# Performance work log

Hardware: AMD Instinct MI355X
Metric: run time of the kernel (lower is better)

Reference implementation:

```python
import jax, jax.numpy as jnp
import numpy as np

LAMBDA = 1.0

def _patches3x3(x):
    # x: [B, C, H, W] -> [B, C, 3, 3, H, W] of 3x3 zero-padded neighborhoods
    B, C, H, W = x.shape
    xp = jnp.pad(x, ((0, 0), (0, 0), (1, 1), (1, 1)))
    rows = []
    for i in range(3):
        cols = [xp[:, :, i:i + H, j:j + W] for j in range(3)]
        rows.append(jnp.stack(cols, axis=2))  # [B, C, 3, H, W]
    return jnp.stack(rows, axis=2)  # [B, C, 3, 3, H, W]


def setup_inputs() -> dict:
    key = jax.random.key(0)
    kU, kV, kW = jax.random.split(key, 3)
    B, Cin, Cout, H, W = 8, 16, 16, 224, 224
    U = jax.random.normal(kU, (B, Cin, H, W), dtype=jnp.float32)
    V = jax.random.normal(kV, (B, Cin, H, W), dtype=jnp.float32)
    # nn.init.uniform_(weight, -0.1, 0.1)
    weight = jax.random.uniform(kW, (Cout, Cin, 3, 3), dtype=jnp.float32,
                                minval=-0.1, maxval=0.1)
    return {"U": U, "V": V, "weight": weight}


def reference(U, V, weight):
    # u1_u2 / v1_v2: 3x3 neighborhood minus center pixel, per input channel
    u_diff = _patches3x3(U) - U[:, :, None, None, :, :]  # [B,C,3,3,H,W]
    v_diff = _patches3x3(V) - V[:, :, None, None, :, :]
    inv_l2 = 1.0 / (LAMBDA * LAMBDA)
    # S = 1 / sqrt(1 + |v1-v2|^2 / lambda^2)
    S = jax.lax.rsqrt(1.0 + v_diff * v_diff * inv_l2)
    # out[b,o,h,w] = sum_{c,ki,kj} weight[o,c,ki,kj] * S * u_diff
    out = jnp.einsum('ocij,bcijhw->bohw', weight, S * u_diff)
    return out
```

## Files before the change

kernel.cpp:

```cpp
#include <hip/hip_runtime.h>


constexpr int Bn = 8, Ci = 16, Co = 16, H = 224, W = 224;
constexpr int HW = H * W;
constexpr int TW = 32, TH = 8;

template <bool EDGE>
__device__ __forceinline__ void load_nbhd(const float* __restrict__ p,
                                          int h, int w, float out9[9]) {
#pragma unroll
  for (int dh = 0; dh < 3; ++dh) {
#pragma unroll
    for (int dw = 0; dw < 3; ++dw) {
      const int k = dh * 3 + dw;
      if (!EDGE) {
        out9[k] = p[(dh - 1) * W + (dw - 1)];
      } else {
        const int hh = h + dh - 1, ww = w + dw - 1;
        const bool ok = ((unsigned)hh < (unsigned)H) & ((unsigned)ww < (unsigned)W);
        const int off = ok ? ((dh - 1) * W + (dw - 1)) : 0;
        const float val = p[off];
        out9[k] = ok ? val : 0.0f;
      }
    }
  }
}

template <bool EDGE>
__device__ __forceinline__ void compute_pixel(
    const float* __restrict__ U, const float* __restrict__ V,
    float* __restrict__ Out, int b, int h, int w,
    const float (*__restrict__ wt)[9][Co]) {
  float acc[Co];
#pragma unroll
  for (int o = 0; o < Co; ++o) acc[o] = 0.0f;

  const size_t pix = (size_t)h * W + w;
  const float* up0 = U + (size_t)b * Ci * HW + pix;
  const float* vp0 = V + (size_t)b * Ci * HW + pix;

  for (int c = 0; c < Ci; ++c) {
    const float* up = up0 + c * HW;
    const float* vp = vp0 + c * HW;
    float u[9], v[9];
    load_nbhd<EDGE>(up, h, w, u);
    load_nbhd<EDGE>(vp, h, w, v);
    const float uc = u[4], vc = v[4];

    float t[9];
#pragma unroll
    for (int k = 0; k < 9; ++k) {
      if (k == 4) continue;
      const float vd = v[k] - vc;
      const float s = rsqrtf(fmaf(vd, vd, 1.0f));
      t[k] = s * (u[k] - uc);
    }

#pragma unroll
    for (int k = 0; k < 9; ++k) {
      if (k == 4) continue;
      const float tk = t[k];
#pragma unroll
      for (int o = 0; o < Co; o += 4) {
        const float4 wv = *reinterpret_cast<const float4*>(&wt[c][k][o]);
        acc[o + 0] = fmaf(wv.x, tk, acc[o + 0]);
        acc[o + 1] = fmaf(wv.y, tk, acc[o + 1]);
        acc[o + 2] = fmaf(wv.z, tk, acc[o + 2]);
        acc[o + 3] = fmaf(wv.w, tk, acc[o + 3]);
      }
    }
  }

  float* op = Out + (size_t)b * Co * HW + pix;
#pragma unroll
  for (int o = 0; o < Co; ++o) op[(size_t)o * HW] = acc[o];
}

__global__ __launch_bounds__(256)
void sdconv_kernel(const float* __restrict__ U, const float* __restrict__ V,
                   const float* __restrict__ Wg, float* __restrict__ Out) {
  __shared__ float wt[Ci][9][Co];
  for (int i = threadIdx.x; i < Co * Ci * 9; i += 256) {
    const int k = i % 9;
    const int c = (i / 9) % Ci;
    const int o = i / (9 * Ci);
    wt[c][k][o] = Wg[i];
  }
  __syncthreads();

  const int tw = threadIdx.x & (TW - 1);
  const int th = threadIdx.x / TW;
  const int w = blockIdx.x * TW + tw;
  const int h = blockIdx.y * TH + th;
  const int b = blockIdx.z;

  const bool edge = (blockIdx.x == 0) | (blockIdx.x == gridDim.x - 1) |
                    (blockIdx.y == 0) | (blockIdx.y == gridDim.y - 1);
  if (edge)
    compute_pixel<true>(U, V, Out, b, h, w, wt);
  else
    compute_pixel<false>(U, V, Out, b, h, w, wt);
}

extern "C" void kernel_launch(void* const* d_in, const int* in_sizes, int n_in,
                              void* d_out, int out_size, void* d_ws, size_t ws_size,
                              hipStream_t stream) {
  const float* U  = (const float*)d_in[0];
  const float* V  = (const float*)d_in[1];
  const float* Wg = (const float*)d_in[2];
  float* Out = (float*)d_out;

  dim3 grid(W / TW, H / TH, Bn);
  dim3 block(TW * TH);
  sdconv_kernel<<<grid, block, 0, stream>>>(U, V, Wg, Out);
}
```

Before: 134.5 us.

## Compute channel-tap contraction with fp16 MFMA and sliding-row neighborhood reuse

Replaces the per-pixel scalar FMA loop over 16 output channels with a 16x16x32 fp16 MFMA per row of pixels. The 8 non-center taps times 4 channels per lane group form the K dimension. Each wave computes 16 pixels by 4 rows, sliding a 3-row window so vertical neighbor loads are reused across rows. Weights are loaded straight from global memory into fp16 B fragments, with no shared-memory staging. This trades fp32 accuracy for fp16 operands and gives a smaller block and tile.

```diff
diff --git a/kernel.cpp b/kernel.cpp
--- a/kernel.cpp
+++ b/kernel.cpp
@@ -3,103 +3,118 @@
 
 constexpr int Bn = 8, Ci = 16, Co = 16, H = 224, W = 224;
 constexpr int HW = H * W;
-constexpr int TW = 32, TH = 8;
+
+typedef _Float16 f16x8 __attribute__((ext_vector_type(8)));
+typedef float    f32x4 __attribute__((ext_vector_type(4)));
 
 template <bool EDGE>
-__device__ __forceinline__ void load_nbhd(const float* __restrict__ p,
-                                          int h, int w, float out9[9]) {
-#pragma unroll
-  for (int dh = 0; dh < 3; ++dh) {
-#pragma unroll
-    for (int dw = 0; dw < 3; ++dw) {
-      const int k = dh * 3 + dw;
-      if (!EDGE) {
-        out9[k] = p[(dh - 1) * W + (dw - 1)];
-      } else {
-        const int hh = h + dh - 1, ww = w + dw - 1;
-        const bool ok = ((unsigned)hh < (unsigned)H) & ((unsigned)ww < (unsigned)W);
-        const int off = ok ? ((dh - 1) * W + (dw - 1)) : 0;
-        const float val = p[off];
-        out9[k] = ok ? val : 0.0f;
-      }
+__device__ __forceinline__ void load_row(const float* __restrict__ plane,
+                                         int h, int w, float r[3]) {
+  if (!EDGE) {
+    const float* q = plane + h * W + w;
+    r[0] = q[-1]; r[1] = q[0]; r[2] = q[1];
+  } else {
+    if ((unsigned)h < (unsigned)H) {
+      const float* q = plane + h * W + w;
+      r[0] = (w >= 1)     ? q[-1] : 0.0f;
+      r[1] = q[0];
+      r[2] = (w + 1 < W) ? q[1] : 0.0f;
+    } else {
+      r[0] = 0.0f; r[1] = 0.0f; r[2] = 0.0f;
     }
   }
 }
 
 template <bool EDGE>
-__device__ __forceinline__ void compute_pixel(
+__device__ __forceinline__ void sdconv_wave(
     const float* __restrict__ U, const float* __restrict__ V,
-    float* __restrict__ Out, int b, int h, int w,
-    const float (*__restrict__ wt)[9][Co]) {
-  float acc[Co];
+    const float* __restrict__ Wg, float* __restrict__ Out,
+    int b, int h0, int w0, int lane) {
+  const int px = lane & 15;
+  const int cg = lane >> 4;
+
+  const int w = w0 + px;
+
+  f16x8 bfrag[4];
 #pragma unroll
-  for (int o = 0; o < Co; ++o) acc[o] = 0.0f;
+  for (int kc = 0; kc < 4; ++kc) {
+    const int c = 4 * kc + cg;
+    const float* wp = Wg + (px * Ci + c) * 9;
+#pragma unroll
+    for (int j = 0; j < 8; ++j) {
+      const int tap = (j < 4) ? j : j + 1;
+      bfrag[kc][j] = (_Float16)wp[tap];
+    }
+  }
 
-  const size_t pix = (size_t)h * W + w;
-  const float* up0 = U + (size_t)b * Ci * HW + pix;
-  const float* vp0 = V + (size_t)b * Ci * HW + pix;
-
-  for (int c = 0; c < Ci; ++c) {
-    const float* up = up0 + c * HW;
-    const float* vp = vp0 + c * HW;
-    float u[9], v[9];
-    load_nbhd<EDGE>(up, h, w, u);
-    load_nbhd<EDGE>(vp, h, w, v);
-    const float uc = u[4], vc = v[4];
-
-    float t[9];
+  f32x4 d[4];
 #pragma unroll
-    for (int k = 0; k < 9; ++k) {
-      if (k == 4) continue;
-      const float vd = v[k] - vc;
-      const float s = rsqrtf(fmaf(vd, vd, 1.0f));
-      t[k] = s * (u[k] - uc);
-    }
+  for (int r = 0; r < 4; ++r) { d[r][0] = 0.f; d[r][1] = 0.f; d[r][2] = 0.f; d[r][3] = 0.f; }
 
 #pragma unroll
-    for (int k = 0; k < 9; ++k) {
-      if (k == 4) continue;
-      const float tk = t[k];
+  for (int kc = 0; kc < 4; ++kc) {
+    const int c = 4 * kc + cg;
+    const float* up = U + ((size_t)(b * Ci + c)) * HW;
+    const float* vp = V + ((size_t)(b * Ci + c)) * HW;
+
+    float u[3][3], v[3][3];
+    load_row<EDGE>(up, h0 - 1, w, u[0]);
+    load_row<EDGE>(vp, h0 - 1, w, v[0]);
+    load_row<EDGE>(up, h0,     w, u[1]);
+    load_row<EDGE>(vp, h0,     w, v[1]);
+
 #pragma unroll
-      for (int o = 0; o < Co; o += 4) {
-        const float4 wv = *reinterpret_cast<const float4*>(&wt[c][k][o]);
-        acc[o + 0] = fmaf(wv.x, tk, acc[o + 0]);
-        acc[o + 1] = fmaf(wv.y, tk, acc[o + 1]);
-        acc[o + 2] = fmaf(wv.z, tk, acc[o + 2]);
-        acc[o + 3] = fmaf(wv.w, tk, acc[o + 3]);
+    for (int r = 0; r < 4; ++r) {
+      load_row<EDGE>(up, h0 + r + 1, w, u[2]);
+      load_row<EDGE>(vp, h0 + r + 1, w, v[2]);
+
+      const float uc = u[1][1], vc = v[1][1];
+      f16x8 a;
+      int j = 0;
+#pragma unroll
+      for (int dh = 0; dh < 3; ++dh) {
+#pragma unroll
+        for (int dw = 0; dw < 3; ++dw) {
+          if (dh == 1 && dw == 1) continue;
+          const float vd = v[dh][dw] - vc;
+          const float s  = rsqrtf(fmaf(vd, vd, 1.0f));
+          a[j++] = (_Float16)(s * (u[dh][dw] - uc));
+        }
+      }
+      d[r] = __builtin_amdgcn_mfma_f32_16x16x32_f16(a, bfrag[kc], d[r], 0, 0, 0);
+
+#pragma unroll
+      for (int i = 0; i < 3; ++i) {
+        u[0][i] = u[1][i]; u[1][i] = u[2][i];
+        v[0][i] = v[1][i]; v[1][i] = v[2][i];
       }
     }
   }
 
-  float* op = Out + (size_t)b * Co * HW + pix;
+  const int wst = w0 + 4 * cg;
+  const int o   = px;
 #pragma unroll
-  for (int o = 0; o < Co; ++o) op[(size_t)o * HW] = acc[o];
+  for (int r = 0; r < 4; ++r) {
+    float* op = Out + (((size_t)b * Co + o) * H + (h0 + r)) * W + wst;
+    *reinterpret_cast<f32x4*>(op) = d[r];
+  }
 }
 
-__global__ __launch_bounds__(256)
-void sdconv_kernel(const float* __restrict__ U, const float* __restrict__ V,
-                   const float* __restrict__ Wg, float* __restrict__ Out) {
-  __shared__ float wt[Ci][9][Co];
-  for (int i = threadIdx.x; i < Co * Ci * 9; i += 256) {
-    const int k = i % 9;
-    const int c = (i / 9) % Ci;
-    const int o = i / (9 * Ci);
-    wt[c][k][o] = Wg[i];
-  }
-  __syncthreads();
-
-  const int tw = threadIdx.x & (TW - 1);
-  const int th = threadIdx.x / TW;
-  const int w = blockIdx.x * TW + tw;
-  const int h = blockIdx.y * TH + th;
-  const int b = blockIdx.z;
+__global__ __launch_bounds__(128)
+void sdconv_mfma(const float* __restrict__ U, const float* __restrict__ V,
+                 const float* __restrict__ Wg, float* __restrict__ Out) {
+  const int lane = threadIdx.x & 63;
+  const int wv   = threadIdx.x >> 6;
+  const int w0 = blockIdx.x * 16;
+  const int h0 = blockIdx.y * 8 + wv * 4;
+  const int b  = blockIdx.z;
 
   const bool edge = (blockIdx.x == 0) | (blockIdx.x == gridDim.x - 1) |
                     (blockIdx.y == 0) | (blockIdx.y == gridDim.y - 1);
   if (edge)
-    compute_pixel<true>(U, V, Out, b, h, w, wt);
+    sdconv_wave<true >(U, V, Wg, Out, b, h0, w0, lane);
   else
-    compute_pixel<false>(U, V, Out, b, h, w, wt);
+    sdconv_wave<false>(U, V, Wg, Out, b, h0, w0, lane);
 }
 
 extern "C" void kernel_launch(void* const* d_in, const int* in_sizes, int n_in,
@@ -110,7 +125,7 @@
   const float* Wg = (const float*)d_in[2];
   float* Out = (float*)d_out;
 
-  dim3 grid(W / TW, H / TH, Bn);
-  dim3 block(TW * TH);
-  sdconv_kernel<<<grid, block, 0, stream>>>(U, V, Wg, Out);
+  dim3 grid(W / 16, H / 8, Bn);
+  dim3 block(128);
+  sdconv_mfma<<<grid, block, 0, stream>>>(U, V, Wg, Out);
 }
```

Result: faster. 125.7 us (-6.5%).
